# Performance work log

Hardware: AMD Instinct MI355X
Metric: run time of the kernel (lower is better)

Reference implementation:

```python
import jax, jax.numpy as jnp
import numpy as np

N = 50000        # nodes
E = 800_000      # edges (avg degree 16)
D_IN, D_HID, D_OUT = 512, 512, 256
P_DROP = 0.5


def setup_inputs() -> dict:
    key = jax.random.key(0)
    k0, k1, k2, k3 = jax.random.split(key, 4)
    x = jax.random.normal(k0, (N, D_IN), dtype=jnp.float32)
    edge_index = jax.random.randint(k1, (2, E), 0, N, dtype=jnp.int64)
    W1 = jax.random.normal(k2, (D_HID, D_IN), dtype=jnp.float32) * 0.02
    b1 = jnp.zeros((D_HID,), dtype=jnp.float32)
    W2 = jax.random.normal(k3, (D_OUT, D_HID), dtype=jnp.float32) * 0.02
    b2 = jnp.zeros((D_OUT,), dtype=jnp.float32)
    return {"x": x, "edge_index": edge_index, "W1": W1, "b1": b1, "W2": W2, "b2": b2}


def _gcn_norm(edge_index, n):
    # add self loops, then symmetric GCN normalization: D^-1/2 (A+I) D^-1/2
    src, dst = edge_index[0], edge_index[1]
    loops = jnp.arange(n, dtype=src.dtype)
    src = jnp.concatenate([src, loops])
    dst = jnp.concatenate([dst, loops])
    deg = jax.ops.segment_sum(jnp.ones_like(src, dtype=jnp.float32), dst, num_segments=n)
    dinv = jax.lax.rsqrt(deg)  # deg >= 1 because of self loops
    norm = dinv[src] * dinv[dst]  # [E+N]
    return src, dst, norm


def _propagate(x, src, dst, norm):
    # out[i] = sum_{(j->i)} norm_e * x[j]
    return jax.ops.segment_sum(x[src] * norm[:, None], dst, num_segments=x.shape[0])


def reference(x, edge_index, W1, b1, W2, b2):
    src, dst, norm = _gcn_norm(edge_index, x.shape[0])
    # SGConv layer 1 (K=1): propagate then linear
    h = _propagate(x, src, dst, norm) @ W1.T + b1
    h = jax.nn.relu(h)
    # F.dropout(p) with training=True default -> deterministic fixed-key mask here
    keep = jax.random.bernoulli(jax.random.key(42), 1.0 - P_DROP, h.shape)
    embedding = jnp.where(keep, h / (1.0 - P_DROP), 0.0)
    # SGConv layer 2
    out = _propagate(embedding, src, dst, norm) @ W2.T + b2
    return embedding, out
```

## Files before the change

### kernel.cpp

```cpp
#include <hip/hip_runtime.h>

typedef unsigned short u16t;
typedef __attribute__((ext_vector_type(8))) short short8;
typedef __attribute__((ext_vector_type(4))) short short4v;
typedef __attribute__((ext_vector_type(4))) float f32x4;
typedef __attribute__((ext_vector_type(4))) unsigned short u16x4;

__device__ __forceinline__ float bf2f(short b) {
  return __uint_as_float(((unsigned)(unsigned short)b) << 16);
}
__device__ __forceinline__ u16t f2bf(float f) {
  unsigned u = __float_as_uint(f);
  u += 0x7FFFu + ((u >> 16) & 1u);
  return (u16t)(u >> 16);
}

__device__ __forceinline__ bool keep_mask(unsigned flat) {
  const unsigned k0 = 0u, k1 = 42u;
  const unsigned k2 = k0 ^ k1 ^ 0x1BD11BDAu;
  unsigned x0 = 0u + k0;
  unsigned x1 = flat + k1;
#define TF_R(r) { x0 += x1; x1 = (x1 << r) | (x1 >> (32 - r)); x1 ^= x0; }
  TF_R(13) TF_R(15) TF_R(26) TF_R(6)  x0 += k1; x1 += k2 + 1u;
  TF_R(17) TF_R(29) TF_R(16) TF_R(24) x0 += k2; x1 += k0 + 2u;
  TF_R(13) TF_R(15) TF_R(26) TF_R(6)  x0 += k0; x1 += k1 + 3u;
  TF_R(17) TF_R(29) TF_R(16) TF_R(24) x0 += k1; x1 += k2 + 4u;
  TF_R(13) TF_R(15) TF_R(26) TF_R(6)  x0 += k2; x1 += k0 + 5u;
#undef TF_R
  return ((x0 ^ x1) >> 31) == 0u;
}

__device__ __forceinline__ void load_lds16(const u16t* g, u16t* l) {
  __builtin_amdgcn_global_load_lds((__attribute__((address_space(1))) void*)g,
                                   (__attribute__((address_space(3))) void*)l,
                                   16, 0, 0);
}

__global__ void cvt_bf16(const float* __restrict__ s, u16t* __restrict__ d, int n) {
  int i = (blockIdx.x * 256 + threadIdx.x) * 4;
  if (i < n) {
    f32x4 v = *(const f32x4*)&s[i];
    u16x4 o = { f2bf(v.x), f2bf(v.y), f2bf(v.z), f2bf(v.w) };
    *(u16x4*)&d[i] = o;
  }
}

__global__ __launch_bounds__(256) void cvt_x_mask(const float* __restrict__ s,
    u16t* __restrict__ d, unsigned* __restrict__ mask, int n, int nwords) {
  int t = blockIdx.x * 256 + threadIdx.x;
  int i = t * 4;
  if (i < n) {
    f32x4 v = *(const f32x4*)&s[i];
    u16x4 o = { f2bf(v.x), f2bf(v.y), f2bf(v.z), f2bf(v.w) };
    *(u16x4*)&d[i] = o;
  }
  if (t < nwords) {
    unsigned base = (unsigned)t * 32u;
    unsigned m = 0u;
    for (int k = 0; k < 32; ++k) m |= (keep_mask(base + (unsigned)k) ? 1u : 0u) << k;
    mask[t] = m;
  }
}

__global__ void count_edges(const int* __restrict__ dst, int E, int* __restrict__ cnt) {
  int e = blockIdx.x * 256 + threadIdx.x;
  if (e < E) atomicAdd(&cnt[dst[e]], 1);
}

__global__ __launch_bounds__(256) void rowp_build(const int* __restrict__ cnt,
    int* __restrict__ rowp, int* __restrict__ cursor, float* __restrict__ dinv,
    int* __restrict__ gctr, int n) {
  __shared__ int sd[256];
  __shared__ int sbase;
  const int tid = threadIdx.x;
  const int i = blockIdx.x * 256 + tid;
  int c = (i < n) ? cnt[i] : 0;
  int v = c;
  sd[tid] = v;
  __syncthreads();
  for (int o = 1; o < 256; o <<= 1) {
    int t = (tid >= o) ? sd[tid - o] : 0;
    __syncthreads();
    v += t;
    sd[tid] = v;
    __syncthreads();
  }
  if (tid == 255) sbase = atomicAdd(gctr, v);
  __syncthreads();
  if (i < n) {
    int start = sbase + v - c;
    rowp[i] = start;
    cursor[i] = start;
    dinv[i] = rsqrtf((float)(c + 1));
  }
}

__global__ void fill_csr(const int* __restrict__ src, const int* __restrict__ dst, int E,
                         int* __restrict__ cursor, u16t* __restrict__ col) {
  int e = blockIdx.x * 256 + threadIdx.x;
  if (e < E) {
    int d = dst[e];
    int pos = atomicAdd(&cursor[d], 1);
    col[pos] = (u16t)src[e];
  }
}

__global__ __launch_bounds__(256) void gemm_bt_sl(const u16t* __restrict__ A,
                                                  const u16t* __restrict__ B,
                                                  u16t* __restrict__ C,
                                                  int K, int Mrows) {
  __shared__ __align__(16) u16t lA[128 * 32];
  __shared__ __align__(16) u16t lB[128 * 32];
  const int tid = threadIdx.x;
  const int wave = tid >> 6, lane = tid & 63;
  const int wm = (wave & 1) * 64, wn = (wave >> 1) * 64;
  const int lrow = lane & 15, lq = lane >> 4;
  const u16t* Ab = A + (size_t)blockIdx.x * 128 * K;
  const u16t* Bb = B + (size_t)blockIdx.y * 128 * K;
  const int r0 = tid >> 2, c0 = (tid & 3) * 8;
  const int ldsOff = __builtin_amdgcn_readfirstlane((tid >> 6) * 512);

  f32x4 acc[4][4];
  const f32x4 zero = {0.f, 0.f, 0.f, 0.f};
#pragma unroll
  for (int mi = 0; mi < 4; ++mi)
#pragma unroll
    for (int ni = 0; ni < 4; ++ni) acc[mi][ni] = zero;

  for (int kt = 0; kt < K; kt += 32) {
    __syncthreads();
    load_lds16(Ab + (size_t)r0 * K + kt + c0, &lA[ldsOff]);
    load_lds16(Ab + (size_t)(r0 + 64) * K + kt + c0, &lA[2048 + ldsOff]);
    load_lds16(Bb + (size_t)r0 * K + kt + c0, &lB[ldsOff]);
    load_lds16(Bb + (size_t)(r0 + 64) * K + kt + c0, &lB[2048 + ldsOff]);
    __syncthreads();
    short8 af[4], bfr[4];
#pragma unroll
    for (int mi = 0; mi < 4; ++mi)
      af[mi] = *(const short8*)&lA[(wm + mi * 16 + lrow) * 32 + lq * 8];
#pragma unroll
    for (int ni = 0; ni < 4; ++ni)
      bfr[ni] = *(const short8*)&lB[(wn + ni * 16 + lrow) * 32 + lq * 8];
#pragma unroll
    for (int mi = 0; mi < 4; ++mi)
#pragma unroll
      for (int ni = 0; ni < 4; ++ni)
        acc[mi][ni] = __builtin_amdgcn_mfma_f32_16x16x32_bf16(af[mi], bfr[ni], acc[mi][ni], 0, 0, 0);
  }

  const int crow0 = blockIdx.x * 128 + wm + lq * 4;
  const int ccol0 = blockIdx.y * 128 + wn + lrow;
#pragma unroll
  for (int mi = 0; mi < 4; ++mi)
#pragma unroll
    for (int r = 0; r < 4; ++r)
#pragma unroll
      for (int ni = 0; ni < 4; ++ni) {
        int cc = ccol0 + ni * 16;
        size_t idx = ((size_t)(cc >> 5) * Mrows + (crow0 + mi * 16 + r)) * 32 + (cc & 31);
        C[idx] = f2bf(acc[mi][ni][r]);
      }
}

__global__ __launch_bounds__(256) void prop1_kernel(const u16t* __restrict__ y1s,
    const u16t* __restrict__ colu, const int* __restrict__ rowp, const int* __restrict__ rowend,
    const float* __restrict__ dinv, const float* __restrict__ b1,
    const unsigned* __restrict__ kmask,
    float* __restrict__ embf, u16t* __restrict__ embb, int n, int Mrows, int chunks) {
  const int t = threadIdx.x;
  const int fl4 = (t & 7) * 4;
  const int bid = blockIdx.x;
  const int half = chunks << 3;
  const int phase = bid >= half;
  const int rem = bid - (phase ? half : 0);
  const int sl = (rem & 7) + (phase << 3);
  const int i = (rem >> 3) * 32 + (t >> 3);
  if (i >= n) return;

  const u16t* T = y1s + (size_t)sl * Mrows * 32;
  const float di = dinv[i];
  float acc[4];
  {
    short4v u = *(const short4v*)&T[(size_t)i * 32 + fl4];
#pragma unroll
    for (int j = 0; j < 4; ++j) acc[j] = di * bf2f(u[j]);
  }
  int e = rowp[i];
  const int e1 = rowend[i];
  for (; e + 4 <= e1; e += 4) {
    const int s0 = (int)colu[e], s1 = (int)colu[e + 1];
    const int s2 = (int)colu[e + 2], s3 = (int)colu[e + 3];
    const float w0 = dinv[s0], w1 = dinv[s1], w2 = dinv[s2], w3 = dinv[s3];
    short4v u0 = *(const short4v*)&T[(size_t)s0 * 32 + fl4];
    short4v u1 = *(const short4v*)&T[(size_t)s1 * 32 + fl4];
    short4v u2 = *(const short4v*)&T[(size_t)s2 * 32 + fl4];
    short4v u3 = *(const short4v*)&T[(size_t)s3 * 32 + fl4];
#pragma unroll
    for (int j = 0; j < 4; ++j) acc[j] += w0 * bf2f(u0[j]);
#pragma unroll
    for (int j = 0; j < 4; ++j) acc[j] += w1 * bf2f(u1[j]);
#pragma unroll
    for (int j = 0; j < 4; ++j) acc[j] += w2 * bf2f(u2[j]);
#pragma unroll
    for (int j = 0; j < 4; ++j) acc[j] += w3 * bf2f(u3[j]);
  }
  for (; e < e1; ++e) {
    const int s = (int)colu[e];
    const float w = dinv[s];
    short4v u = *(const short4v*)&T[(size_t)s * 32 + fl4];
#pragma unroll
    for (int j = 0; j < 4; ++j) acc[j] += w * bf2f(u[j]);
  }

  const int f = sl * 32 + fl4;
  const unsigned km = kmask[i * 16 + sl];
  f32x4 o;
  short4v ob;
#pragma unroll
  for (int j = 0; j < 4; ++j) {
    float h = di * acc[j] + b1[f + j];
    h = fmaxf(h, 0.f);
    float eb = ((km >> (fl4 + j)) & 1u) ? 2.f * h : 0.f;
    o[j] = eb;
    ob[j] = (short)f2bf(eb);
  }
  __builtin_nontemporal_store(o, (f32x4*)&embf[(size_t)i * 512 + f]);
  __builtin_nontemporal_store(ob, (short4v*)&embb[(size_t)i * 512 + f]);
}

__global__ __launch_bounds__(256) void prop2_kernel(const u16t* __restrict__ zs,
    const u16t* __restrict__ colu, const int* __restrict__ rowp, const int* __restrict__ rowend,
    const float* __restrict__ dinv, const float* __restrict__ b2,
    float* __restrict__ outp, int n, int Mrows, int chunks) {
  const int t = threadIdx.x;
  const int fl4 = (t & 7) * 4;
  const int bid = blockIdx.x;
  const int sl = bid & 7;
  const int i = (bid >> 3) * 32 + (t >> 3);
  (void)chunks;
  if (i >= n) return;

  const u16t* T = zs + (size_t)sl * Mrows * 32;
  const float di = dinv[i];
  float acc[4];
  {
    short4v u = *(const short4v*)&T[(size_t)i * 32 + fl4];
#pragma unroll
    for (int j = 0; j < 4; ++j) acc[j] = di * bf2f(u[j]);
  }
  int e = rowp[i];
  const int e1 = rowend[i];
  for (; e + 4 <= e1; e += 4) {
    const int s0 = (int)colu[e], s1 = (int)colu[e + 1];
    const int s2 = (int)colu[e + 2], s3 = (int)colu[e + 3];
    const float w0 = dinv[s0], w1 = dinv[s1], w2 = dinv[s2], w3 = dinv[s3];
    short4v u0 = *(const short4v*)&T[(size_t)s0 * 32 + fl4];
    short4v u1 = *(const short4v*)&T[(size_t)s1 * 32 + fl4];
    short4v u2 = *(const short4v*)&T[(size_t)s2 * 32 + fl4];
    short4v u3 = *(const short4v*)&T[(size_t)s3 * 32 + fl4];
#pragma unroll
    for (int j = 0; j < 4; ++j) acc[j] += w0 * bf2f(u0[j]);
#pragma unroll
    for (int j = 0; j < 4; ++j) acc[j] += w1 * bf2f(u1[j]);
#pragma unroll
    for (int j = 0; j < 4; ++j) acc[j] += w2 * bf2f(u2[j]);
#pragma unroll
    for (int j = 0; j < 4; ++j) acc[j] += w3 * bf2f(u3[j]);
  }
  for (; e < e1; ++e) {
    const int s = (int)colu[e];
    const float w = dinv[s];
    short4v u = *(const short4v*)&T[(size_t)s * 32 + fl4];
#pragma unroll
    for (int j = 0; j < 4; ++j) acc[j] += w * bf2f(u[j]);
  }

  const int f = sl * 32 + fl4;
  f32x4 o;
#pragma unroll
  for (int j = 0; j < 4; ++j) o[j] = di * acc[j] + b2[f + j];
  __builtin_nontemporal_store(o, (f32x4*)&outp[(size_t)i * 256 + f]);
}

extern "C" void kernel_launch(void* const* d_in, const int* in_sizes, int n_in,
                              void* d_out, int out_size, void* d_ws, size_t ws_size,
                              hipStream_t stream) {
  (void)n_in; (void)out_size; (void)ws_size;
  const float* x  = (const float*)d_in[0];
  const int*   ei = (const int*)d_in[1];
  const float* W1 = (const float*)d_in[2];
  const float* b1 = (const float*)d_in[3];
  const float* W2 = (const float*)d_in[4];
  const float* b2 = (const float*)d_in[5];

  const int Nn = in_sizes[0] / 512;
  const int E  = in_sizes[1] / 2;
  const int Mpad = ((Nn + 127) / 128) * 128;
  const int K = 512;
  const int CH = (Nn + 31) / 32;

  char* ws = (char*)d_ws;
  size_t off = 0;
  auto take = [&](size_t bytes) -> char* {
    char* p = ws + off;
    off += (bytes + 255) & ~(size_t)255;
    return p;
  };
  u16t* xb   = (u16t*)take((size_t)Mpad * 512 * 2);
  u16t* y1s  = (u16t*)take((size_t)16 * Mpad * 32 * 2);
  u16t* W1b  = (u16t*)take((size_t)512 * 512 * 2);
  u16t* W2b  = (u16t*)take((size_t)256 * 512 * 2);
  int*   cnt    = (int*)take((size_t)(Nn + 1) * 4);
  int*   rowp   = (int*)take((size_t)Nn * 4);
  int*   cursor = (int*)take((size_t)Nn * 4);
  float* dinv   = (float*)take((size_t)Nn * 4);
  u16t*  colu   = (u16t*)take((size_t)E * 2);
  unsigned* kmask = (unsigned*)take((size_t)Nn * 16 * 4);

  float* embf = (float*)d_out;
  float* outf = (float*)d_out + (size_t)Nn * 512;

  hipMemsetAsync(cnt, 0, (size_t)(Nn + 1) * 4, stream);

  const int n1 = Nn * 512;
  cvt_x_mask<<<(n1 / 4 + 255) / 256, 256, 0, stream>>>(x, xb, kmask, n1, Nn * 16);
  cvt_bf16<<<(512 * 512 / 4 + 255) / 256, 256, 0, stream>>>(W1, W1b, 512 * 512);
  cvt_bf16<<<(256 * 512 / 4 + 255) / 256, 256, 0, stream>>>(W2, W2b, 256 * 512);

  count_edges<<<(E + 255) / 256, 256, 0, stream>>>(ei + E, E, cnt);
  rowp_build<<<(Nn + 255) / 256, 256, 0, stream>>>(cnt, rowp, cursor, dinv, cnt + Nn, Nn);
  fill_csr<<<(E + 255) / 256, 256, 0, stream>>>(ei, ei + E, E, cursor, colu);

  dim3 g1(Mpad / 128, 4);
  gemm_bt_sl<<<g1, 256, 0, stream>>>(xb, W1b, y1s, K, Mpad);
  prop1_kernel<<<16 * CH, 256, 0, stream>>>(y1s, colu, rowp, cursor, dinv, b1, kmask,
                                            embf, xb , Nn, Mpad, CH);

  u16t* zs = y1s;
  dim3 g2(Mpad / 128, 2);
  gemm_bt_sl<<<g2, 256, 0, stream>>>(xb, W2b, zs, K, Mpad);
  prop2_kernel<<<8 * CH, 256, 0, stream>>>(zs, colu, rowp, cursor, dinv, b2, outf, Nn, Mpad, CH);
}
```

Measured before the change: 664.4 us.

## Fold source-side dinv scaling into GEMM epilogue and prefetch CSR indices

The GEMM epilogue now multiplies each output row by dinv[row] before writing bf16, so the propagation kernels no longer gather dinv per neighbor or scale the self term by it; only the final di scaling remains. The gather loops are also restructured to load 8 column indices ahead (software pipelining) while accumulating the previous 8 rows. This removes one dependent random load per edge and raises memory-level parallelism, at the cost of extra registers and rounding the pre-scaled values to bf16.

Measured after the change: 603.4 us. 1.1x faster.

```diff
diff --git a/kernel.cpp b/kernel.cpp
--- a/kernel.cpp
+++ b/kernel.cpp
@@ -108,7 +108,9 @@
 __global__ __launch_bounds__(256) void gemm_bt_sl(const u16t* __restrict__ A,
                                                   const u16t* __restrict__ B,
                                                   u16t* __restrict__ C,
-                                                  int K, int Mrows) {
+                                                  int K, int Mrows,
+                                                  const float* __restrict__ dinv,
+                                                  int Nclamp) {
   __shared__ __align__(16) u16t lA[128 * 32];
   __shared__ __align__(16) u16t lB[128 * 32];
   const int tid = threadIdx.x;
@@ -153,13 +155,16 @@
 #pragma unroll
   for (int mi = 0; mi < 4; ++mi)
 #pragma unroll
-    for (int r = 0; r < 4; ++r)
+    for (int r = 0; r < 4; ++r) {
+      const int row = crow0 + mi * 16 + r;
+      const float dr = dinv[row < Nclamp ? row : 0];
 #pragma unroll
       for (int ni = 0; ni < 4; ++ni) {
         int cc = ccol0 + ni * 16;
-        size_t idx = ((size_t)(cc >> 5) * Mrows + (crow0 + mi * 16 + r)) * 32 + (cc & 31);
-        C[idx] = f2bf(acc[mi][ni][r]);
+        size_t idx = ((size_t)(cc >> 5) * Mrows + row) * 32 + (cc & 31);
+        C[idx] = f2bf(dr * acc[mi][ni][r]);
       }
+    }
 }
 
 __global__ __launch_bounds__(256) void prop1_kernel(const u16t* __restrict__ y1s,
@@ -177,39 +182,46 @@
   const int i = (rem >> 3) * 32 + (t >> 3);
   if (i >= n) return;
 
-  const u16t* T = y1s + (size_t)sl * Mrows * 32;
+  const u16t* T = y1s + (size_t)sl * Mrows * 32 + fl4;
   const float di = dinv[i];
   float acc[4];
   {
-    short4v u = *(const short4v*)&T[(size_t)i * 32 + fl4];
-#pragma unroll
-    for (int j = 0; j < 4; ++j) acc[j] = di * bf2f(u[j]);
+    short4v u = *(const short4v*)&T[(size_t)i * 32];
+#pragma unroll
+    for (int j = 0; j < 4; ++j) acc[j] = bf2f(u[j]);
   }
   int e = rowp[i];
   const int e1 = rowend[i];
-  for (; e + 4 <= e1; e += 4) {
-    const int s0 = (int)colu[e], s1 = (int)colu[e + 1];
-    const int s2 = (int)colu[e + 2], s3 = (int)colu[e + 3];
-    const float w0 = dinv[s0], w1 = dinv[s1], w2 = dinv[s2], w3 = dinv[s3];
-    short4v u0 = *(const short4v*)&T[(size_t)s0 * 32 + fl4];
-    short4v u1 = *(const short4v*)&T[(size_t)s1 * 32 + fl4];
-    short4v u2 = *(const short4v*)&T[(size_t)s2 * 32 + fl4];
-    short4v u3 = *(const short4v*)&T[(size_t)s3 * 32 + fl4];
-#pragma unroll
-    for (int j = 0; j < 4; ++j) acc[j] += w0 * bf2f(u0[j]);
-#pragma unroll
-    for (int j = 0; j < 4; ++j) acc[j] += w1 * bf2f(u1[j]);
-#pragma unroll
-    for (int j = 0; j < 4; ++j) acc[j] += w2 * bf2f(u2[j]);
-#pragma unroll
-    for (int j = 0; j < 4; ++j) acc[j] += w3 * bf2f(u3[j]);
+  if (e + 8 <= e1) {
+    int c[8];
+#pragma unroll
+    for (int q = 0; q < 8; ++q) c[q] = (int)colu[e + q];
+    e += 8;
+    while (e + 8 <= e1) {
+      int c2[8];
+#pragma unroll
+      for (int q = 0; q < 8; ++q) c2[q] = (int)colu[e + q];
+#pragma unroll
+      for (int q = 0; q < 8; ++q) {
+        short4v u = *(const short4v*)&T[(size_t)c[q] * 32];
+#pragma unroll
+        for (int j = 0; j < 4; ++j) acc[j] += bf2f(u[j]);
+      }
+#pragma unroll
+      for (int q = 0; q < 8; ++q) c[q] = c2[q];
+      e += 8;
+    }
+#pragma unroll
+    for (int q = 0; q < 8; ++q) {
+      short4v u = *(const short4v*)&T[(size_t)c[q] * 32];
+#pragma unroll
+      for (int j = 0; j < 4; ++j) acc[j] += bf2f(u[j]);
+    }
   }
   for (; e < e1; ++e) {
-    const int s = (int)colu[e];
-    const float w = dinv[s];
-    short4v u = *(const short4v*)&T[(size_t)s * 32 + fl4];
-#pragma unroll
-    for (int j = 0; j < 4; ++j) acc[j] += w * bf2f(u[j]);
+    short4v u = *(const short4v*)&T[(size_t)(int)colu[e] * 32];
+#pragma unroll
+    for (int j = 0; j < 4; ++j) acc[j] += bf2f(u[j]);
   }
 
   const int f = sl * 32 + fl4;
@@ -240,39 +252,46 @@
   (void)chunks;
   if (i >= n) return;
 
-  const u16t* T = zs + (size_t)sl * Mrows * 32;
+  const u16t* T = zs + (size_t)sl * Mrows * 32 + fl4;
   const float di = dinv[i];
   float acc[4];
   {
-    short4v u = *(const short4v*)&T[(size_t)i * 32 + fl4];
-#pragma unroll
-    for (int j = 0; j < 4; ++j) acc[j] = di * bf2f(u[j]);
+    short4v u = *(const short4v*)&T[(size_t)i * 32];
+#pragma unroll
+    for (int j = 0; j < 4; ++j) acc[j] = bf2f(u[j]);
   }
   int e = rowp[i];
   const int e1 = rowend[i];
-  for (; e + 4 <= e1; e += 4) {
-    const int s0 = (int)colu[e], s1 = (int)colu[e + 1];
-    const int s2 = (int)colu[e + 2], s3 = (int)colu[e + 3];
-    const float w0 = dinv[s0], w1 = dinv[s1], w2 = dinv[s2], w3 = dinv[s3];
-    short4v u0 = *(const short4v*)&T[(size_t)s0 * 32 + fl4];
-    short4v u1 = *(const short4v*)&T[(size_t)s1 * 32 + fl4];
-    short4v u2 = *(const short4v*)&T[(size_t)s2 * 32 + fl4];
-    short4v u3 = *(const short4v*)&T[(size_t)s3 * 32 + fl4];
-#pragma unroll
-    for (int j = 0; j < 4; ++j) acc[j] += w0 * bf2f(u0[j]);
-#pragma unroll
-    for (int j = 0; j < 4; ++j) acc[j] += w1 * bf2f(u1[j]);
-#pragma unroll
-    for (int j = 0; j < 4; ++j) acc[j] += w2 * bf2f(u2[j]);
-#pragma unroll
-    for (int j = 0; j < 4; ++j) acc[j] += w3 * bf2f(u3[j]);
+  if (e + 8 <= e1) {
+    int c[8];
+#pragma unroll
+    for (int q = 0; q < 8; ++q) c[q] = (int)colu[e + q];
+    e += 8;
+    while (e + 8 <= e1) {
+      int c2[8];
+#pragma unroll
+      for (int q = 0; q < 8; ++q) c2[q] = (int)colu[e + q];
+#pragma unroll
+      for (int q = 0; q < 8; ++q) {
+        short4v u = *(const short4v*)&T[(size_t)c[q] * 32];
+#pragma unroll
+        for (int j = 0; j < 4; ++j) acc[j] += bf2f(u[j]);
+      }
+#pragma unroll
+      for (int q = 0; q < 8; ++q) c[q] = c2[q];
+      e += 8;
+    }
+#pragma unroll
+    for (int q = 0; q < 8; ++q) {
+      short4v u = *(const short4v*)&T[(size_t)c[q] * 32];
+#pragma unroll
+      for (int j = 0; j < 4; ++j) acc[j] += bf2f(u[j]);
+    }
   }
   for (; e < e1; ++e) {
-    const int s = (int)colu[e];
-    const float w = dinv[s];
-    short4v u = *(const short4v*)&T[(size_t)s * 32 + fl4];
-#pragma unroll
-    for (int j = 0; j < 4; ++j) acc[j] += w * bf2f(u[j]);
+    short4v u = *(const short4v*)&T[(size_t)(int)colu[e] * 32];
+#pragma unroll
+    for (int j = 0; j < 4; ++j) acc[j] += bf2f(u[j]);
   }
 
   const int f = sl * 32 + fl4;
@@ -332,12 +351,12 @@
   fill_csr<<<(E + 255) / 256, 256, 0, stream>>>(ei, ei + E, E, cursor, colu);
 
   dim3 g1(Mpad / 128, 4);
-  gemm_bt_sl<<<g1, 256, 0, stream>>>(xb, W1b, y1s, K, Mpad);
+  gemm_bt_sl<<<g1, 256, 0, stream>>>(xb, W1b, y1s, K, Mpad, dinv, Nn);
   prop1_kernel<<<16 * CH, 256, 0, stream>>>(y1s, colu, rowp, cursor, dinv, b1, kmask,
                                             embf, xb , Nn, Mpad, CH);
 
   u16t* zs = y1s;
   dim3 g2(Mpad / 128, 2);
-  gemm_bt_sl<<<g2, 256, 0, stream>>>(xb, W2b, zs, K, Mpad);
+  gemm_bt_sl<<<g2, 256, 0, stream>>>(xb, W2b, zs, K, Mpad, dinv, Nn);
   prop2_kernel<<<8 * CH, 256, 0, stream>>>(zs, colu, rowp, cursor, dinv, b2, outf, Nn, Mpad, CH);
 }
```
